# Performance work log

Hardware: AMD Instinct MI355X
Metric: run time of the kernel (lower is better)

The kernel has to match this reference:

```python
import jax, jax.numpy as jnp
import numpy as np

B, N, DIN, DOUT, L = 32, 512, 768, 256, 512
NEG = -9.0e15
SLOPE = 0.2  # LeakyReLU negative slope


def setup_inputs() -> dict:
    key = jax.random.key(0)
    ks = jax.random.split(key, 7)
    h = jax.random.normal(ks[0], (B, N, DIN), dtype=jnp.float32)
    adj = jax.random.randint(ks[1], (B, N, N), 0, 2, dtype=jnp.int32)
    positions = jax.random.randint(ks[2], (B, N), 0, L, dtype=jnp.int32)
    W = jax.random.normal(ks[3], (DIN, DOUT), dtype=jnp.float32) * 0.02
    a1 = jax.random.normal(ks[4], (DOUT,), dtype=jnp.float32) * 0.02
    a2 = jax.random.normal(ks[5], (DOUT,), dtype=jnp.float32) * 0.02
    pos_table = jax.random.normal(ks[6], (L, DOUT), dtype=jnp.float32) * 0.02
    return {"h": h, "adj": adj, "positions": positions, "W": W,
            "a1": a1, "a2": a2, "pos_table": pos_table}


def reference(h, adj, positions, W, a1, a2, pos_table):
    # Wh = W(h) + pos_emb(positions)   -> [B, N, DOUT]
    Wh = jnp.einsum('bnd,de->bne', h, W) + pos_table[positions]
    # Pairwise GAT score: e_ij = leakyrelu(a1 . Wh_i + a2 . Wh_j)
    # (identical math to concat([Wh_i, Wh_j]) @ [a1; a2], without the O(N^2*2D) tensor)
    s1 = jnp.einsum('bnd,d->bn', Wh, a1)  # source term   [B, N]
    s2 = jnp.einsum('bnd,d->bn', Wh, a2)  # target term   [B, N]
    e = jax.nn.leaky_relu(s1[:, :, None] + s2[:, None, :], negative_slope=SLOPE)  # [B,N,N]
    # adjacency mask + softmax over neighbors (dropout is identity in eval)
    attention = jax.nn.softmax(jnp.where(adj > 0, e, NEG), axis=-1)  # [B, N, N]
    h_prime = jnp.einsum('bij,bjd->bid', attention, Wh)  # [B, N, DOUT]
    return h_prime, attention
```

## Files before the change

### kernel.cpp

```cpp
#include <hip/hip_runtime.h>
#include <math.h>

#define B 32
#define N 512
#define DIN 768
#define DOUT 256
#define NEGV -9.0e15f
#define SLOPE 0.2f

typedef __bf16 bf16x8 __attribute__((ext_vector_type(8)));
typedef float f32x4 __attribute__((ext_vector_type(4)));
typedef unsigned short us8 __attribute__((ext_vector_type(8)));

__device__ __forceinline__ unsigned short f2b(float f) {
    union { float f; unsigned u; } v; v.f = f;
    unsigned r = v.u + 0x7FFF + ((v.u >> 16) & 1);
    return (unsigned short)(r >> 16);
}

__device__ __forceinline__ float b2f(unsigned short h) {
    union { unsigned u; float f; } v; v.u = ((unsigned)h) << 16;
    return v.f;
}

__device__ __forceinline__ void gload_lds16(const unsigned short* g, unsigned short* l) {
    __builtin_amdgcn_global_load_lds(
        (const __attribute__((address_space(1))) unsigned int*)(unsigned long long)(uintptr_t)g,
        (__attribute__((address_space(3))) unsigned int*)(uintptr_t)l,
        16, 0, 0);
}

__global__ __launch_bounds__(256) void conv_fused(
    const float4* __restrict__ hin, ushort4* __restrict__ hout,
    const float* __restrict__ W, unsigned short* __restrict__ WT) {
    __shared__ unsigned short tile[64][65];
    const int t = threadIdx.x;
    if (blockIdx.x < 12288) {
        int idx = blockIdx.x * 256 + t;
        float4 v = hin[idx];
        ushort4 o;
        o.x = f2b(v.x); o.y = f2b(v.y); o.z = f2b(v.z); o.w = f2b(v.w);
        hout[idx] = o;
    } else {
        int bid = blockIdx.x - 12288;
        int k0 = (bid % 12) * 64, n0 = (bid / 12) * 64;
        const int cl = t & 63, cg = t >> 6;
#pragma unroll
        for (int i = 0; i < 16; ++i) {
            int k = cg * 16 + i;
            tile[cl][k] = f2b(W[(size_t)(k0 + k) * DOUT + n0 + cl]);
        }
        __syncthreads();
#pragma unroll
        for (int i = 0; i < 16; ++i) {
            int n = cg * 16 + i;
            WT[(size_t)(n0 + n) * DIN + k0 + cl] = tile[n][cl];
        }
    }
}

__global__ __launch_bounds__(256) void wh_mfma(
    const unsigned short* __restrict__ hA,
    const unsigned short* __restrict__ WT,
    const int*   __restrict__ pos,
    const float* __restrict__ ptab,
    const float* __restrict__ a1,
    const float* __restrict__ a2,
    unsigned short* __restrict__ WhT,
    float* __restrict__ s1, float* __restrict__ s2)
{
    constexpr int K = DIN;
    __shared__ unsigned short smem[12288];
    unsigned short* As = smem;
    unsigned short* Bs = smem + 8192;
    unsigned short* tileT = smem;

    const int t    = threadIdx.x;
    const int lane = t & 63;
    const int w    = t >> 6;
    const int lin  = blockIdx.x;
    const int m0   = (lin & 127) * 128;
    const int n0   = (lin >> 7) * 64;

    int arow[4], apos[4];
#pragma unroll
    for (int i = 0; i < 4; ++i) {
        int c = i * 256 + t;
        arow[i] = c >> 3;
        apos[i] = (c & 7) ^ ((c >> 3) & 7);
    }
    int brow[2], bpos[2];
#pragma unroll
    for (int i = 0; i < 2; ++i) {
        int c = i * 256 + t;
        brow[i] = c >> 3;
        bpos[i] = (c & 7) ^ ((c >> 3) & 7);
    }
    const unsigned short* gA[4];
    const unsigned short* gB[2];
#pragma unroll
    for (int i = 0; i < 4; ++i) gA[i] = hA + (size_t)(m0 + arow[i]) * K + apos[i] * 8;
#pragma unroll
    for (int i = 0; i < 2; ++i) gB[i] = WT + (size_t)(n0 + brow[i]) * K + bpos[i] * 8;
    unsigned short* lA[4];
    unsigned short* lB[2];
#pragma unroll
    for (int i = 0; i < 4; ++i) lA[i] = As + (i * 256 + (t & 192)) * 8;
#pragma unroll
    for (int i = 0; i < 2; ++i) lB[i] = Bs + (i * 256 + (t & 192)) * 8;

    const int wm = (w & 1) * 64, wn = (w >> 1) * 32;
    const int l15 = lane & 15, q = lane >> 4;
    int aoff[2][4], boff[2][2];
#pragma unroll
    for (int kk = 0; kk < 2; ++kk) {
        int pg = kk * 4 + q;
#pragma unroll
        for (int i = 0; i < 4; ++i) {
            int rm = wm + i * 16 + l15;
            aoff[kk][i] = rm * 64 + ((pg ^ (rm & 7)) * 8);
        }
#pragma unroll
        for (int i = 0; i < 2; ++i) {
            int rn = wn + i * 16 + l15;
            boff[kk][i] = rn * 64 + ((pg ^ (rn & 7)) * 8);
        }
    }

    f32x4 acc[4][2];
#pragma unroll
    for (int i = 0; i < 4; ++i)
#pragma unroll
        for (int j = 0; j < 2; ++j) acc[i][j] = (f32x4){0.f, 0.f, 0.f, 0.f};

    for (int k0 = 0; k0 < K; k0 += 64) {
#pragma unroll
        for (int i = 0; i < 4; ++i) gload_lds16(gA[i] + k0, lA[i]);
#pragma unroll
        for (int i = 0; i < 2; ++i) gload_lds16(gB[i] + k0, lB[i]);
        __syncthreads();
#pragma unroll
        for (int kk = 0; kk < 2; ++kk) {
            bf16x8 af[4], bfr[2];
#pragma unroll
            for (int i = 0; i < 4; ++i) af[i] = *(const bf16x8*)(As + aoff[kk][i]);
#pragma unroll
            for (int i = 0; i < 2; ++i) bfr[i] = *(const bf16x8*)(Bs + boff[kk][i]);
#pragma unroll
            for (int mi = 0; mi < 4; ++mi)
#pragma unroll
                for (int ni = 0; ni < 2; ++ni)
                    acc[mi][ni] = __builtin_amdgcn_mfma_f32_16x16x32_bf16(
                        af[mi], bfr[ni], acc[mi][ni], 0, 0, 0);
        }
        __syncthreads();
    }

    const float a1v[2] = { a1[n0 + wn + l15], a1[n0 + wn + 16 + l15] };
    const float a2v[2] = { a2[n0 + wn + l15], a2[n0 + wn + 16 + l15] };
#pragma unroll
    for (int mi = 0; mi < 4; ++mi) {
        const int jb = wm + mi * 16 + q * 4;
        float v[2][4];
#pragma unroll
        for (int ni = 0; ni < 2; ++ni) {
            const int nl = wn + ni * 16 + l15;
            ushort4 pk;
            unsigned short* pp = (unsigned short*)&pk;
#pragma unroll
            for (int r = 0; r < 4; ++r) {
                int m = m0 + jb + r;
                int p = pos[m];
                float val = acc[mi][ni][r] + ptab[(size_t)p * DOUT + n0 + nl];
                v[ni][r] = val;
                pp[r] = f2b(val);
            }
            *(ushort4*)&tileT[nl * 136 + jb] = pk;
        }
#pragma unroll
        for (int r = 0; r < 4; ++r) {
            float t1 = v[0][r] * a1v[0] + v[1][r] * a1v[1];
            float t2 = v[0][r] * a2v[0] + v[1][r] * a2v[1];
#pragma unroll
            for (int mk = 1; mk < 16; mk <<= 1) {
                t1 += __shfl_xor(t1, mk);
                t2 += __shfl_xor(t2, mk);
            }
            if (l15 == 0) {
                atomicAdd(&s1[m0 + jb + r], t1);
                atomicAdd(&s2[m0 + jb + r], t2);
            }
        }
    }
    __syncthreads();
    const int bb = m0 >> 9, j0 = m0 & 511;
#pragma unroll
    for (int rr = 0; rr < 4; ++rr) {
        int nl = (t >> 4) + rr * 16;
        int jl = (t & 15) * 8;
        us8 vv = *(const us8*)&tileT[nl * 136 + jl];
        *(us8*)&WhT[((size_t)bb * DOUT + n0 + nl) * N + j0 + jl] = vv;
    }
}

__global__ __launch_bounds__(256) void attn_softmax(
    const float* __restrict__ s1,
    const float* __restrict__ s2,
    const int*   __restrict__ adj,
    float*       __restrict__ att,
    unsigned int* __restrict__ attb)
{
    const int row = blockIdx.x;
    const int b   = row >> 9;
    const int t   = threadIdx.x;

    const float s1i = s1[row];
    const float2 s2p = ((const float2*)(s2 + b * N))[t];
    const int2   ap  = ((const int2*)(adj + (size_t)row * N))[t];

    float v0 = s1i + s2p.x; v0 = v0 > 0.f ? v0 : SLOPE * v0;
    float v1 = s1i + s2p.y; v1 = v1 > 0.f ? v1 : SLOPE * v1;
    v0 = (ap.x > 0) ? v0 : NEGV;
    v1 = (ap.y > 0) ? v1 : NEGV;

    __shared__ float red[4];
    __shared__ float bcast;

    float m = fmaxf(v0, v1);
#pragma unroll
    for (int off = 32; off > 0; off >>= 1)
        m = fmaxf(m, __shfl_down(m, off));
    const int wid = t >> 6;
    if ((t & 63) == 0) red[wid] = m;
    __syncthreads();
    if (t == 0) bcast = fmaxf(fmaxf(red[0], red[1]), fmaxf(red[2], red[3]));
    __syncthreads();
    m = bcast;

    float p0 = __expf(v0 - m);
    float p1 = __expf(v1 - m);
    float s = p0 + p1;
#pragma unroll
    for (int off = 32; off > 0; off >>= 1)
        s += __shfl_down(s, off);
    __syncthreads();
    if ((t & 63) == 0) red[wid] = s;
    __syncthreads();
    if (t == 0) bcast = red[0] + red[1] + red[2] + red[3];
    __syncthreads();
    const float inv = 1.0f / bcast;

    float o0 = p0 * inv, o1 = p1 * inv;
    ((float2*)(att + (size_t)row * N))[t] = (float2){o0, o1};
    attb[(size_t)row * 256 + t] = (unsigned)f2b(o0) | ((unsigned)f2b(o1) << 16);
}

__global__ __launch_bounds__(256) void hp_mfma(
    const unsigned short* __restrict__ attb,
    const unsigned short* __restrict__ WhT,
    float* __restrict__ hp)
{
    constexpr int K = N;
    __shared__ unsigned short smem[12288];
    unsigned short* As = smem;
    unsigned short* Bs = smem + 8192;

    const int t    = threadIdx.x;
    const int lane = t & 63;
    const int w    = t >> 6;
    const int lin  = blockIdx.x;
    const int n0   = (lin >> 7) * 64;
    const int rest = lin & 127;
    const int bb   = rest >> 2;
    const int m0   = (rest & 3) * 128;

    const unsigned short* A  = attb + (size_t)bb * N * N;
    const unsigned short* Bg = WhT  + (size_t)bb * DOUT * N;

    int arow[4], apos[4];
#pragma unroll
    for (int i = 0; i < 4; ++i) {
        int c = i * 256 + t;
        arow[i] = c >> 3;
        apos[i] = (c & 7) ^ ((c >> 3) & 7);
    }
    int brow[2], bpos[2];
#pragma unroll
    for (int i = 0; i < 2; ++i) {
        int c = i * 256 + t;
        brow[i] = c >> 3;
        bpos[i] = (c & 7) ^ ((c >> 3) & 7);
    }
    const unsigned short* gA[4];
    const unsigned short* gB[2];
#pragma unroll
    for (int i = 0; i < 4; ++i) gA[i] = A + (size_t)(m0 + arow[i]) * K + apos[i] * 8;
#pragma unroll
    for (int i = 0; i < 2; ++i) gB[i] = Bg + (size_t)(n0 + brow[i]) * K + bpos[i] * 8;
    unsigned short* lA[4];
    unsigned short* lB[2];
#pragma unroll
    for (int i = 0; i < 4; ++i) lA[i] = As + (i * 256 + (t & 192)) * 8;
#pragma unroll
    for (int i = 0; i < 2; ++i) lB[i] = Bs + (i * 256 + (t & 192)) * 8;

    const int wm = (w & 1) * 64, wn = (w >> 1) * 32;
    const int l15 = lane & 15, q = lane >> 4;
    int aoff[2][4], boff[2][2];
#pragma unroll
    for (int kk = 0; kk < 2; ++kk) {
        int pg = kk * 4 + q;
#pragma unroll
        for (int i = 0; i < 4; ++i) {
            int rm = wm + i * 16 + l15;
            aoff[kk][i] = rm * 64 + ((pg ^ (rm & 7)) * 8);
        }
#pragma unroll
        for (int i = 0; i < 2; ++i) {
            int rn = wn + i * 16 + l15;
            boff[kk][i] = rn * 64 + ((pg ^ (rn & 7)) * 8);
        }
    }

    f32x4 acc[4][2];
#pragma unroll
    for (int i = 0; i < 4; ++i)
#pragma unroll
        for (int j = 0; j < 2; ++j) acc[i][j] = (f32x4){0.f, 0.f, 0.f, 0.f};

    for (int k0 = 0; k0 < K; k0 += 64) {
#pragma unroll
        for (int i = 0; i < 4; ++i) gload_lds16(gA[i] + k0, lA[i]);
#pragma unroll
        for (int i = 0; i < 2; ++i) gload_lds16(gB[i] + k0, lB[i]);
        __syncthreads();
#pragma unroll
        for (int kk = 0; kk < 2; ++kk) {
            bf16x8 af[4], bfr[2];
#pragma unroll
            for (int i = 0; i < 4; ++i) af[i] = *(const bf16x8*)(As + aoff[kk][i]);
#pragma unroll
            for (int i = 0; i < 2; ++i) bfr[i] = *(const bf16x8*)(Bs + boff[kk][i]);
#pragma unroll
            for (int mi = 0; mi < 4; ++mi)
#pragma unroll
                for (int ni = 0; ni < 2; ++ni)
                    acc[mi][ni] = __builtin_amdgcn_mfma_f32_16x16x32_bf16(
                        af[mi], bfr[ni], acc[mi][ni], 0, 0, 0);
        }
        __syncthreads();
    }

#pragma unroll
    for (int mi = 0; mi < 4; ++mi) {
#pragma unroll
        for (int r = 0; r < 4; ++r) {
            int m = m0 + wm + mi * 16 + q * 4 + r;
#pragma unroll
            for (int ni = 0; ni < 2; ++ni) {
                int n = n0 + wn + ni * 16 + l15;
                hp[((size_t)bb * N + m) * DOUT + n] = acc[mi][ni][r];
            }
        }
    }
}

extern "C" void kernel_launch(void* const* d_in, const int* in_sizes, int n_in,
                              void* d_out, int out_size, void* d_ws, size_t ws_size,
                              hipStream_t stream) {
    const float* h         = (const float*)d_in[0];
    const int*   adj       = (const int*)  d_in[1];
    const int*   positions = (const int*)  d_in[2];
    const float* W         = (const float*)d_in[3];
    const float* a1        = (const float*)d_in[4];
    const float* a2        = (const float*)d_in[5];
    const float* pos_table = (const float*)d_in[6];

    float* out     = (float*)d_out;
    float* h_prime = out;
    float* att     = out + (size_t)B * N * DOUT;

    char* ws = (char*)d_ws;
    unsigned short* h_bf  = (unsigned short*)ws;
    unsigned short* attb  = (unsigned short*)ws;
    unsigned short* WT    = (unsigned short*)(ws + 25165824);
    unsigned short* WhT   = (unsigned short*)(ws + 25559040);
    float*          s1    = (float*)(ws + 33947648);
    float*          s2    = s1 + (size_t)B * N;

    hipMemsetAsync(s1, 0, (size_t)2 * B * N * sizeof(float), stream);
    conv_fused<<<12288 + 48, 256, 0, stream>>>((const float4*)h, (ushort4*)h_bf, W, WT);
    wh_mfma<<<512, 256, 0, stream>>>(h_bf, WT, positions, pos_table, a1, a2, WhT, s1, s2);
    attn_softmax<<<B * N, 256, 0, stream>>>(s1, s2, adj, att, (unsigned int*)attb);
    hp_mfma<<<512, 256, 0, stream>>>(attb, WhT, h_prime);
}
```

Baseline: 172.0 us.

## Fuse softmax into attention GEMM and convert fp32 input inside Wh GEMM

Drops the separate fp32→bf16 conversion pass over h. The Wh GEMM now reads fp32 rows straight from global memory into registers, converts them in place and skips LDS staging. The softmax and attention@Wh kernels become one kernel: each block computes 64 softmax rows, writes fp32 attention and keeps bf16 probabilities in swizzled LDS, then runs the MFMA GEMM against WhT. This removes the bf16 h and attention round-trips through global memory. In exchange, the 64 KB LDS P buffer and 512-thread blocks give low occupancy, and the unstaged global loads in the GEMMs may be less efficient.

```diff
diff --git a/kernel.cpp b/kernel.cpp
--- a/kernel.cpp
+++ b/kernel.cpp
@@ -18,49 +18,34 @@
     return (unsigned short)(r >> 16);
 }
 
-__device__ __forceinline__ float b2f(unsigned short h) {
-    union { unsigned u; float f; } v; v.u = ((unsigned)h) << 16;
-    return v.f;
-}
-
-__device__ __forceinline__ void gload_lds16(const unsigned short* g, unsigned short* l) {
-    __builtin_amdgcn_global_load_lds(
-        (const __attribute__((address_space(1))) unsigned int*)(unsigned long long)(uintptr_t)g,
-        (__attribute__((address_space(3))) unsigned int*)(uintptr_t)l,
-        16, 0, 0);
-}
-
-__global__ __launch_bounds__(256) void conv_fused(
-    const float4* __restrict__ hin, ushort4* __restrict__ hout,
-    const float* __restrict__ W, unsigned short* __restrict__ WT) {
+__device__ __forceinline__ bf16x8 cvt8(float4 a, float4 b) {
+    bf16x8 v;
+    v[0] = (__bf16)a.x; v[1] = (__bf16)a.y; v[2] = (__bf16)a.z; v[3] = (__bf16)a.w;
+    v[4] = (__bf16)b.x; v[5] = (__bf16)b.y; v[6] = (__bf16)b.z; v[7] = (__bf16)b.w;
+    return v;
+}
+
+__global__ __launch_bounds__(256) void conv_wt(const float* __restrict__ W,
+                                               unsigned short* __restrict__ WT) {
     __shared__ unsigned short tile[64][65];
+    const int k0 = blockIdx.x * 64, n0 = blockIdx.y * 64;
     const int t = threadIdx.x;
-    if (blockIdx.x < 12288) {
-        int idx = blockIdx.x * 256 + t;
-        float4 v = hin[idx];
-        ushort4 o;
-        o.x = f2b(v.x); o.y = f2b(v.y); o.z = f2b(v.z); o.w = f2b(v.w);
-        hout[idx] = o;
-    } else {
-        int bid = blockIdx.x - 12288;
-        int k0 = (bid % 12) * 64, n0 = (bid / 12) * 64;
-        const int cl = t & 63, cg = t >> 6;
-#pragma unroll
-        for (int i = 0; i < 16; ++i) {
-            int k = cg * 16 + i;
-            tile[cl][k] = f2b(W[(size_t)(k0 + k) * DOUT + n0 + cl]);
-        }
-        __syncthreads();
-#pragma unroll
-        for (int i = 0; i < 16; ++i) {
-            int n = cg * 16 + i;
-            WT[(size_t)(n0 + n) * DIN + k0 + cl] = tile[n][cl];
-        }
+    const int cl = t & 63, cg = t >> 6;
+#pragma unroll
+    for (int i = 0; i < 16; ++i) {
+        int k = cg * 16 + i;
+        tile[cl][k] = f2b(W[(size_t)(k0 + k) * DOUT + n0 + cl]);
+    }
+    __syncthreads();
+#pragma unroll
+    for (int i = 0; i < 16; ++i) {
+        int n = cg * 16 + i;
+        WT[(size_t)(n0 + n) * DIN + k0 + cl] = tile[n][cl];
     }
 }
 
 __global__ __launch_bounds__(256) void wh_mfma(
-    const unsigned short* __restrict__ hA,
+    const float* __restrict__ hA,
     const unsigned short* __restrict__ WT,
     const int*   __restrict__ pos,
     const float* __restrict__ ptab,
@@ -70,10 +55,7 @@
     float* __restrict__ s1, float* __restrict__ s2)
 {
     constexpr int K = DIN;
-    __shared__ unsigned short smem[12288];
-    unsigned short* As = smem;
-    unsigned short* Bs = smem + 8192;
-    unsigned short* tileT = smem;
+    __shared__ unsigned short tileT[64 * 136];
 
     const int t    = threadIdx.x;
     const int lane = t & 63;
@@ -82,50 +64,17 @@
     const int m0   = (lin & 127) * 128;
     const int n0   = (lin >> 7) * 64;
 
-    int arow[4], apos[4];
-#pragma unroll
-    for (int i = 0; i < 4; ++i) {
-        int c = i * 256 + t;
-        arow[i] = c >> 3;
-        apos[i] = (c & 7) ^ ((c >> 3) & 7);
-    }
-    int brow[2], bpos[2];
-#pragma unroll
-    for (int i = 0; i < 2; ++i) {
-        int c = i * 256 + t;
-        brow[i] = c >> 3;
-        bpos[i] = (c & 7) ^ ((c >> 3) & 7);
-    }
-    const unsigned short* gA[4];
-    const unsigned short* gB[2];
-#pragma unroll
-    for (int i = 0; i < 4; ++i) gA[i] = hA + (size_t)(m0 + arow[i]) * K + apos[i] * 8;
-#pragma unroll
-    for (int i = 0; i < 2; ++i) gB[i] = WT + (size_t)(n0 + brow[i]) * K + bpos[i] * 8;
-    unsigned short* lA[4];
-    unsigned short* lB[2];
-#pragma unroll
-    for (int i = 0; i < 4; ++i) lA[i] = As + (i * 256 + (t & 192)) * 8;
-#pragma unroll
-    for (int i = 0; i < 2; ++i) lB[i] = Bs + (i * 256 + (t & 192)) * 8;
-
     const int wm = (w & 1) * 64, wn = (w >> 1) * 32;
     const int l15 = lane & 15, q = lane >> 4;
-    int aoff[2][4], boff[2][2];
-#pragma unroll
-    for (int kk = 0; kk < 2; ++kk) {
-        int pg = kk * 4 + q;
-#pragma unroll
-        for (int i = 0; i < 4; ++i) {
-            int rm = wm + i * 16 + l15;
-            aoff[kk][i] = rm * 64 + ((pg ^ (rm & 7)) * 8);
-        }
-#pragma unroll
-        for (int i = 0; i < 2; ++i) {
-            int rn = wn + i * 16 + l15;
-            boff[kk][i] = rn * 64 + ((pg ^ (rn & 7)) * 8);
-        }
-    }
+
+    const float* aRow[4];
+#pragma unroll
+    for (int mi = 0; mi < 4; ++mi)
+        aRow[mi] = hA + (size_t)(m0 + wm + mi * 16 + l15) * DIN + q * 8;
+    const unsigned short* bRow[2];
+#pragma unroll
+    for (int ni = 0; ni < 2; ++ni)
+        bRow[ni] = WT + (size_t)(n0 + wn + ni * 16 + l15) * DIN + q * 8;
 
     f32x4 acc[4][2];
 #pragma unroll
@@ -133,27 +82,23 @@
 #pragma unroll
         for (int j = 0; j < 2; ++j) acc[i][j] = (f32x4){0.f, 0.f, 0.f, 0.f};
 
-    for (int k0 = 0; k0 < K; k0 += 64) {
-#pragma unroll
-        for (int i = 0; i < 4; ++i) gload_lds16(gA[i] + k0, lA[i]);
-#pragma unroll
-        for (int i = 0; i < 2; ++i) gload_lds16(gB[i] + k0, lB[i]);
-        __syncthreads();
-#pragma unroll
-        for (int kk = 0; kk < 2; ++kk) {
-            bf16x8 af[4], bfr[2];
-#pragma unroll
-            for (int i = 0; i < 4; ++i) af[i] = *(const bf16x8*)(As + aoff[kk][i]);
-#pragma unroll
-            for (int i = 0; i < 2; ++i) bfr[i] = *(const bf16x8*)(Bs + boff[kk][i]);
-#pragma unroll
-            for (int mi = 0; mi < 4; ++mi)
-#pragma unroll
-                for (int ni = 0; ni < 2; ++ni)
-                    acc[mi][ni] = __builtin_amdgcn_mfma_f32_16x16x32_bf16(
-                        af[mi], bfr[ni], acc[mi][ni], 0, 0, 0);
-        }
-        __syncthreads();
+#pragma unroll 4
+    for (int k0 = 0; k0 < K; k0 += 32) {
+        bf16x8 af[4], bfr[2];
+#pragma unroll
+        for (int mi = 0; mi < 4; ++mi) {
+            const float4* ap = (const float4*)(aRow[mi] + k0);
+            af[mi] = cvt8(ap[0], ap[1]);
+        }
+#pragma unroll
+        for (int ni = 0; ni < 2; ++ni)
+            bfr[ni] = *(const bf16x8*)(bRow[ni] + k0);
+#pragma unroll
+        for (int mi = 0; mi < 4; ++mi)
+#pragma unroll
+            for (int ni = 0; ni < 2; ++ni)
+                acc[mi][ni] = __builtin_amdgcn_mfma_f32_16x16x32_bf16(
+                    af[mi], bfr[ni], acc[mi][ni], 0, 0, 0);
     }
 
     const float a1v[2] = { a1[n0 + wn + l15], a1[n0 + wn + 16 + l15] };
@@ -203,123 +148,82 @@
     }
 }
 
-__global__ __launch_bounds__(256) void attn_softmax(
+__global__ __launch_bounds__(512) void attn_hp(
     const float* __restrict__ s1,
     const float* __restrict__ s2,
     const int*   __restrict__ adj,
-    float*       __restrict__ att,
-    unsigned int* __restrict__ attb)
-{
-    const int row = blockIdx.x;
-    const int b   = row >> 9;
-    const int t   = threadIdx.x;
-
-    const float s1i = s1[row];
-    const float2 s2p = ((const float2*)(s2 + b * N))[t];
-    const int2   ap  = ((const int2*)(adj + (size_t)row * N))[t];
-
-    float v0 = s1i + s2p.x; v0 = v0 > 0.f ? v0 : SLOPE * v0;
-    float v1 = s1i + s2p.y; v1 = v1 > 0.f ? v1 : SLOPE * v1;
-    v0 = (ap.x > 0) ? v0 : NEGV;
-    v1 = (ap.y > 0) ? v1 : NEGV;
-
-    __shared__ float red[4];
-    __shared__ float bcast;
-
-    float m = fmaxf(v0, v1);
-#pragma unroll
-    for (int off = 32; off > 0; off >>= 1)
-        m = fmaxf(m, __shfl_down(m, off));
-    const int wid = t >> 6;
-    if ((t & 63) == 0) red[wid] = m;
-    __syncthreads();
-    if (t == 0) bcast = fmaxf(fmaxf(red[0], red[1]), fmaxf(red[2], red[3]));
-    __syncthreads();
-    m = bcast;
-
-    float p0 = __expf(v0 - m);
-    float p1 = __expf(v1 - m);
-    float s = p0 + p1;
-#pragma unroll
-    for (int off = 32; off > 0; off >>= 1)
-        s += __shfl_down(s, off);
-    __syncthreads();
-    if ((t & 63) == 0) red[wid] = s;
-    __syncthreads();
-    if (t == 0) bcast = red[0] + red[1] + red[2] + red[3];
-    __syncthreads();
-    const float inv = 1.0f / bcast;
-
-    float o0 = p0 * inv, o1 = p1 * inv;
-    ((float2*)(att + (size_t)row * N))[t] = (float2){o0, o1};
-    attb[(size_t)row * 256 + t] = (unsigned)f2b(o0) | ((unsigned)f2b(o1) << 16);
-}
-
-__global__ __launch_bounds__(256) void hp_mfma(
-    const unsigned short* __restrict__ attb,
     const unsigned short* __restrict__ WhT,
+    float* __restrict__ att,
     float* __restrict__ hp)
 {
-    constexpr int K = N;
-    __shared__ unsigned short smem[12288];
-    unsigned short* As = smem;
-    unsigned short* Bs = smem + 8192;
+    __shared__ unsigned short P[64 * 512];
 
     const int t    = threadIdx.x;
     const int lane = t & 63;
     const int w    = t >> 6;
-    const int lin  = blockIdx.x;
-    const int n0   = (lin >> 7) * 64;
-    const int rest = lin & 127;
-    const int bb   = rest >> 2;
-    const int m0   = (rest & 3) * 128;
-
-    const unsigned short* A  = attb + (size_t)bb * N * N;
-    const unsigned short* Bg = WhT  + (size_t)bb * DOUT * N;
-
-    int arow[4], apos[4];
-#pragma unroll
-    for (int i = 0; i < 4; ++i) {
-        int c = i * 256 + t;
-        arow[i] = c >> 3;
-        apos[i] = (c & 7) ^ ((c >> 3) & 7);
-    }
-    int brow[2], bpos[2];
-#pragma unroll
-    for (int i = 0; i < 2; ++i) {
-        int c = i * 256 + t;
-        brow[i] = c >> 3;
-        bpos[i] = (c & 7) ^ ((c >> 3) & 7);
-    }
-    const unsigned short* gA[4];
-    const unsigned short* gB[2];
-#pragma unroll
-    for (int i = 0; i < 4; ++i) gA[i] = A + (size_t)(m0 + arow[i]) * K + apos[i] * 8;
-#pragma unroll
-    for (int i = 0; i < 2; ++i) gB[i] = Bg + (size_t)(n0 + brow[i]) * K + bpos[i] * 8;
-    unsigned short* lA[4];
-    unsigned short* lB[2];
-#pragma unroll
-    for (int i = 0; i < 4; ++i) lA[i] = As + (i * 256 + (t & 192)) * 8;
-#pragma unroll
-    for (int i = 0; i < 2; ++i) lB[i] = Bs + (i * 256 + (t & 192)) * 8;
-
-    const int wm = (w & 1) * 64, wn = (w >> 1) * 32;
+    const int bb   = blockIdx.x >> 3;
+    const int m0   = (blockIdx.x & 7) * 64;
+
+    {
+        const int r = t >> 3, c = t & 7;
+        const size_t rowg = (size_t)bb * N + m0 + r;
+        const float s1i = s1[rowg];
+        const int4*   adjp = (const int4*)(adj + rowg * N + c * 64);
+        const float4* s2p  = (const float4*)(s2 + (size_t)bb * N + c * 64);
+        float fe[64];
+        float mx = -3.0e38f;
+#pragma unroll
+        for (int i = 0; i < 16; ++i) {
+            int4 a = adjp[i];
+            float4 sv = s2p[i];
+            float v0 = s1i + sv.x; v0 = v0 > 0.f ? v0 : SLOPE * v0; v0 = (a.x > 0) ? v0 : NEGV;
+            float v1 = s1i + sv.y; v1 = v1 > 0.f ? v1 : SLOPE * v1; v1 = (a.y > 0) ? v1 : NEGV;
+            float v2 = s1i + sv.z; v2 = v2 > 0.f ? v2 : SLOPE * v2; v2 = (a.z > 0) ? v2 : NEGV;
+            float v3 = s1i + sv.w; v3 = v3 > 0.f ? v3 : SLOPE * v3; v3 = (a.w > 0) ? v3 : NEGV;
+            fe[i * 4 + 0] = v0; fe[i * 4 + 1] = v1;
+            fe[i * 4 + 2] = v2; fe[i * 4 + 3] = v3;
+            mx = fmaxf(mx, fmaxf(fmaxf(v0, v1), fmaxf(v2, v3)));
+        }
+#pragma unroll
+        for (int mk = 1; mk < 8; mk <<= 1) mx = fmaxf(mx, __shfl_xor(mx, mk));
+        float sum = 0.f;
+#pragma unroll
+        for (int k = 0; k < 64; ++k) { fe[k] = __expf(fe[k] - mx); sum += fe[k]; }
+#pragma unroll
+        for (int mk = 1; mk < 8; mk <<= 1) sum += __shfl_xor(sum, mk);
+        const float inv = 1.0f / sum;
+
+        float* attrow = att + rowg * N + c * 64;
+#pragma unroll
+        for (int i = 0; i < 16; ++i) {
+            float4 o = { fe[i * 4 + 0] * inv, fe[i * 4 + 1] * inv,
+                         fe[i * 4 + 2] * inv, fe[i * 4 + 3] * inv };
+            ((float4*)attrow)[i] = o;
+        }
+#pragma unroll
+        for (int jj = 0; jj < 8; ++jj) {
+            int slot = c * 8 + jj;
+            int S = slot ^ (r & 7) ^ c;
+            bf16x8 pv;
+#pragma unroll
+            for (int e = 0; e < 8; ++e) pv[e] = (__bf16)(fe[jj * 8 + e] * inv);
+            *(bf16x8*)&P[r * 512 + S * 8] = pv;
+        }
+    }
+    __syncthreads();
+
+    const int wn  = w * 32;
     const int l15 = lane & 15, q = lane >> 4;
-    int aoff[2][4], boff[2][2];
-#pragma unroll
-    for (int kk = 0; kk < 2; ++kk) {
-        int pg = kk * 4 + q;
-#pragma unroll
-        for (int i = 0; i < 4; ++i) {
-            int rm = wm + i * 16 + l15;
-            aoff[kk][i] = rm * 64 + ((pg ^ (rm & 7)) * 8);
-        }
-#pragma unroll
-        for (int i = 0; i < 2; ++i) {
-            int rn = wn + i * 16 + l15;
-            boff[kk][i] = rn * 64 + ((pg ^ (rn & 7)) * 8);
-        }
+    const unsigned short* bRow[2];
+#pragma unroll
+    for (int ni = 0; ni < 2; ++ni)
+        bRow[ni] = WhT + ((size_t)bb * DOUT + wn + ni * 16 + l15) * N + q * 8;
+    int rm7[4], rmBase[4];
+#pragma unroll
+    for (int mi = 0; mi < 4; ++mi) {
+        int rm = mi * 16 + l15;
+        rm7[mi] = rm & 7;
+        rmBase[mi] = rm * 512;
     }
 
     f32x4 acc[4][2];
@@ -328,38 +232,36 @@
 #pragma unroll
         for (int j = 0; j < 2; ++j) acc[i][j] = (f32x4){0.f, 0.f, 0.f, 0.f};
 
-    for (int k0 = 0; k0 < K; k0 += 64) {
-#pragma unroll
-        for (int i = 0; i < 4; ++i) gload_lds16(gA[i] + k0, lA[i]);
-#pragma unroll
-        for (int i = 0; i < 2; ++i) gload_lds16(gB[i] + k0, lB[i]);
-        __syncthreads();
-#pragma unroll
-        for (int kk = 0; kk < 2; ++kk) {
-            bf16x8 af[4], bfr[2];
-#pragma unroll
-            for (int i = 0; i < 4; ++i) af[i] = *(const bf16x8*)(As + aoff[kk][i]);
-#pragma unroll
-            for (int i = 0; i < 2; ++i) bfr[i] = *(const bf16x8*)(Bs + boff[kk][i]);
-#pragma unroll
-            for (int mi = 0; mi < 4; ++mi)
-#pragma unroll
-                for (int ni = 0; ni < 2; ++ni)
-                    acc[mi][ni] = __builtin_amdgcn_mfma_f32_16x16x32_bf16(
-                        af[mi], bfr[ni], acc[mi][ni], 0, 0, 0);
-        }
-        __syncthreads();
+#pragma unroll 4
+    for (int k0 = 0; k0 < N; k0 += 32) {
+        const int slot = (k0 >> 3) + q;
+        const int hi = slot >> 3;
+        bf16x8 af[4], bfr[2];
+#pragma unroll
+        for (int ni = 0; ni < 2; ++ni)
+            bfr[ni] = *(const bf16x8*)(bRow[ni] + k0);
+#pragma unroll
+        for (int mi = 0; mi < 4; ++mi) {
+            int S = slot ^ rm7[mi] ^ hi;
+            af[mi] = *(const bf16x8*)&P[rmBase[mi] + S * 8];
+        }
+#pragma unroll
+        for (int mi = 0; mi < 4; ++mi)
+#pragma unroll
+            for (int ni = 0; ni < 2; ++ni)
+                acc[mi][ni] = __builtin_amdgcn_mfma_f32_16x16x32_bf16(
+                    af[mi], bfr[ni], acc[mi][ni], 0, 0, 0);
     }
 
 #pragma unroll
     for (int mi = 0; mi < 4; ++mi) {
 #pragma unroll
-        for (int r = 0; r < 4; ++r) {
-            int m = m0 + wm + mi * 16 + q * 4 + r;
+        for (int rr = 0; rr < 4; ++rr) {
+            int m = m0 + mi * 16 + q * 4 + rr;
 #pragma unroll
             for (int ni = 0; ni < 2; ++ni) {
-                int n = n0 + wn + ni * 16 + l15;
-                hp[((size_t)bb * N + m) * DOUT + n] = acc[mi][ni][r];
+                int n = wn + ni * 16 + l15;
+                hp[((size_t)bb * N + m) * DOUT + n] = acc[mi][ni][rr];
             }
         }
     }
@@ -381,16 +283,16 @@
     float* att     = out + (size_t)B * N * DOUT;
 
     char* ws = (char*)d_ws;
-    unsigned short* h_bf  = (unsigned short*)ws;
-    unsigned short* attb  = (unsigned short*)ws;
-    unsigned short* WT    = (unsigned short*)(ws + 25165824);
-    unsigned short* WhT   = (unsigned short*)(ws + 25559040);
-    float*          s1    = (float*)(ws + 33947648);
-    float*          s2    = s1 + (size_t)B * N;
+    unsigned short* WT  = (unsigned short*)ws;
+    unsigned short* WhT = (unsigned short*)(ws + 0x100000);
+    float*          s1  = (float*)(ws + 0x900000);
+    float*          s2  = s1 + (size_t)B * N;
 
     hipMemsetAsync(s1, 0, (size_t)2 * B * N * sizeof(float), stream);
-    conv_fused<<<12288 + 48, 256, 0, stream>>>((const float4*)h, (ushort4*)h_bf, W, WT);
-    wh_mfma<<<512, 256, 0, stream>>>(h_bf, WT, positions, pos_table, a1, a2, WhT, s1, s2);
-    attn_softmax<<<B * N, 256, 0, stream>>>(s1, s2, adj, att, (unsigned int*)attb);
-    hp_mfma<<<512, 256, 0, stream>>>(attb, WhT, h_prime);
-}
+    {
+        dim3 grid(DIN / 64, DOUT / 64);
+        conv_wt<<<grid, 256, 0, stream>>>(W, WT);
+    }
+    wh_mfma<<<512, 256, 0, stream>>>(h, WT, positions, pos_table, a1, a2, WhT, s1, s2);
+    attn_hp<<<256, 512, 0, stream>>>(s1, s2, adj, WhT, att, h_prime);
+}
```

Result: slower. 208.8 us (+21.4%).
